# Optimization experiments

Measured on AMD Instinct MI355X. Metric: run time of the kernel, lower is better.

The kernel has to match this reference:

```python
import jax, jax.numpy as jnp
import numpy as np

N_NODES = 50000
N_EDGES = 800000
IN_DIM = 128
HID = 128
N_GRAPHS = 64


def setup_inputs() -> dict:
    key = jax.random.key(0)
    ks = jax.random.split(key, 12)
    edge_index = jax.random.randint(ks[0], (2, N_EDGES), 0, N_NODES, dtype=jnp.int64)
    edge_weight = jax.random.uniform(ks[1], (N_EDGES,), dtype=jnp.float32)
    input_feature = jax.random.normal(ks[2], (N_NODES, IN_DIM), dtype=jnp.float32)
    graph_indicator = jnp.sort(jax.random.randint(ks[3], (N_NODES,), 0, N_GRAPHS, dtype=jnp.int64))
    s = 0.05
    W1 = jax.random.normal(ks[4], (IN_DIM, HID), dtype=jnp.float32) * s
    b1 = jnp.zeros((HID,), jnp.float32)
    W2 = jax.random.normal(ks[5], (HID, HID), dtype=jnp.float32) * s
    b2 = jnp.zeros((HID,), jnp.float32)
    W3 = jax.random.normal(ks[6], (HID, HID), dtype=jnp.float32) * s
    b3 = jnp.zeros((HID,), jnp.float32)
    wa = jax.random.normal(ks[7], (3 * HID, 1), dtype=jnp.float32) * s
    ba = jnp.zeros((1,), jnp.float32)
    Wf = jax.random.normal(ks[8], (3 * HID * 2, IN_DIM), dtype=jnp.float32) * s
    bf = jnp.zeros((IN_DIM,), jnp.float32)
    return dict(edge_index=edge_index, edge_weight=edge_weight,
                input_feature=input_feature, graph_indicator=graph_indicator,
                W1=W1, b1=b1, W2=W2, b2=b2, W3=W3, b3=b3,
                wa=wa, ba=ba, Wf=Wf, bf=bf)


def reference(edge_index, edge_weight, input_feature, graph_indicator,
              W1, b1, W2, b2, W3, b3, wa, ba, Wf, bf):
    src, dst = edge_index[0], edge_index[1]

    def gcn(x, W, b):
        # GraphConvolution: adj @ (x @ W) + b, adj given as weighted edge list
        support = x @ W  # [N, d_out]
        msg = edge_weight[:, None] * support[src]  # [E, d_out] gather
        return jax.ops.segment_sum(msg, dst, num_segments=N_NODES) + b

    g1 = jax.nn.relu(gcn(input_feature, W1, b1))
    g2 = jax.nn.relu(gcn(g1, W2, b2))
    g3 = jax.nn.relu(gcn(g2, W3, b3))
    h = jnp.concatenate([g1, g2, g3], axis=1)  # [N, 3*HID]

    # SelfAttentionPooling: attention score via a 1-dim GraphConvolution, tanh gate
    score = jnp.tanh(gcn(h, wa, ba))  # [N, 1]
    pool = h * score

    # segment avg / max pooling per graph
    seg_sum = jax.ops.segment_sum(pool, graph_indicator, num_segments=N_GRAPHS)
    counts = jax.ops.segment_sum(jnp.ones((N_NODES, 1), pool.dtype), graph_indicator,
                                 num_segments=N_GRAPHS)
    avg = seg_sum / jnp.maximum(counts, 1.0)
    mx = jax.ops.segment_max(pool, graph_indicator, num_segments=N_GRAPHS)
    pooled = jnp.concatenate([avg, mx], axis=1)  # [G, 6*HID]

    return jax.nn.relu(pooled @ Wf + bf)  # [G, IN_DIM]
```

## Files before the change

### kernel.cpp

```cpp
#include <hip/hip_runtime.h>
#include <math.h>

#define HID 128
#define POOL_SEG 16
#define WT_STRIDE 136
#define ELL_D 48
#define SC_CHUNK 2048
#define FXS 16384.0f
#define FXI (1.0f/16384.0f)

typedef __attribute__((ext_vector_type(8))) short short8;
typedef __attribute__((ext_vector_type(4))) float float4v;

__device__ inline short f2bf(float f) {
  unsigned u = __builtin_bit_cast(unsigned, f);
  unsigned r = (u + 0x7fff + ((u >> 16) & 1)) >> 16;
  return (short)r;
}
__device__ inline unsigned pack2bf(float lo, float hi) {
  return (unsigned)(unsigned short)f2bf(lo) | ((unsigned)(unsigned short)f2bf(hi) << 16);
}
__device__ inline float bflo(unsigned u) { return __builtin_bit_cast(float, u << 16); }
__device__ inline float bfhi(unsigned u) { return __builtin_bit_cast(float, u & 0xffff0000u); }
__device__ inline float bf2f(unsigned short s) { return __builtin_bit_cast(float, (unsigned)s << 16); }
__device__ inline unsigned short f2h(float f) {
  _Float16 h = (_Float16)f;
  return __builtin_bit_cast(unsigned short, h);
}
__device__ inline float h2f(unsigned short hb) {
  return (float)__builtin_bit_cast(_Float16, hb);
}

__global__ __launch_bounds__(256) void prologue(
    const void* __restrict__ ei_raw, const float* __restrict__ ew,
    int2* __restrict__ packed,
    const float* __restrict__ W1, const float* __restrict__ W2, const float* __restrict__ W3,
    short* __restrict__ T1, short* __restrict__ T2, short* __restrict__ T3,
    const void* __restrict__ gi_raw, int* __restrict__ gstart,
    int E, int N, int G, int EB) {
  int b = blockIdx.x, t = threadIdx.x;
  if (b < EB) {
    int e = b * 256 + t;
    if (e < E) {
      const int* pw = (const int*)ei_raw;
      int nz = 0;
#pragma unroll
      for (int i = 1; i < 64; i += 2) nz |= pw[i];
      int s, d;
      if (nz == 0) {
        const long long* p = (const long long*)ei_raw;
        s = (int)p[e]; d = (int)p[E + e];
      } else {
        const int* p = (const int*)ei_raw;
        s = p[e]; d = p[E + e];
      }
      packed[e] = make_int2((d << 16) | s, __builtin_bit_cast(int, ew[e]));
    }
  } else if (b < EB + 192) {
    int i = (b - EB) * 256 + t;
    int which = i >> 14, idx = i & 16383;
    int k = idx >> 7, nn = idx & 127;
    const float* W = (which == 0) ? W1 : ((which == 1) ? W2 : W3);
    short* T = (which == 0) ? T1 : ((which == 1) ? T2 : T3);
    T[nn * WT_STRIDE + k] = f2bf(W[idx]);
  } else {
    int g = t;
    if (g > G) return;
    if (g == G) { gstart[g] = N; return; }
    bool is64 = (((const int*)gi_raw)[N - 1] == 0);
    const long long* g64 = (const long long*)gi_raw;
    const int* g32 = (const int*)gi_raw;
    int lo = 0, hi = N;
    while (lo < hi) {
      int mid = (lo + hi) >> 1;
      long long v = is64 ? g64[mid] : (long long)g32[mid];
      if (v < (long long)g) lo = mid + 1; else hi = mid;
    }
    gstart[g] = lo;
  }
}

__global__ void scatter_ell(const int2* __restrict__ packed, int* __restrict__ cursor,
                            unsigned* __restrict__ ell, int E, int N) {
  int group = blockIdx.x & 7;
  int chunk = blockIdx.x >> 3;
  int rng = (N + 7) >> 3;
  int lo = group * rng;
  int hi = lo + rng; if (hi > N) hi = N;
  int base = chunk * SC_CHUNK;
  for (int i = 0; i < SC_CHUNK; i += 256) {
    int e = base + i + threadIdx.x;
    if (e < E) {
      int2 rec = packed[e];
      int d = ((unsigned)rec.x) >> 16;
      if (d >= lo && d < hi) {
        unsigned s = (unsigned)rec.x & 0xFFFFu;
        unsigned short wh = f2h(__builtin_bit_cast(float, rec.y));
        int pos = atomicAdd(&cursor[d], 1);
        if (pos < ELL_D)
          ell[(size_t)d * ELL_D + pos] = (s << 16) | (unsigned)wh;
      }
    }
  }
}

__global__ __launch_bounds__(256) void hist_k(const int* __restrict__ cursor,
                                              int* __restrict__ hist_blk, int n, int nb) {
  __shared__ int lh[ELL_D + 1];
  int t = threadIdx.x;
  if (t <= ELL_D) lh[t] = 0;
  __syncthreads();
  int i = blockIdx.x * 256 + t;
  if (i < n) {
    int d = cursor[i]; if (d > ELL_D) d = ELL_D;
    atomicAdd(&lh[d], 1);
  }
  __syncthreads();
  if (t <= ELL_D) hist_blk[t * nb + blockIdx.x] = lh[t];
}

__global__ __launch_bounds__(64) void scan_k(int* __restrict__ hist_blk, int nb) {
  __shared__ int tot[ELL_D + 1];
  __shared__ int base_s[ELL_D + 1];
  int b = threadIdx.x;
  if (b <= ELL_D) {
    int s = 0;
#pragma unroll 8
    for (int k = 0; k < nb; k++) s += hist_blk[b * nb + k];
    tot[b] = s;
  }
  __syncthreads();
  if (b == 0) {
    int r = 0;
    for (int d = 0; d <= ELL_D; d++) { base_s[d] = r; r += tot[d]; }
  }
  __syncthreads();
  if (b <= ELL_D) {
    int r = base_s[b];
#pragma unroll 8
    for (int k = 0; k < nb; k++) {
      int c = hist_blk[b * nb + k];
      hist_blk[b * nb + k] = r;
      r += c;
    }
  }
}

__global__ __launch_bounds__(256) void gemm_mfma(const float* __restrict__ Af,
                                                 const unsigned short* __restrict__ Abf,
                                                 const short* __restrict__ Wt,
                                                 unsigned short* __restrict__ C,
                                                 int n, int a_is_bf16, int gemm_nb,
                                                 const int* __restrict__ deg,
                                                 const int* __restrict__ hist_blk,
                                                 int* __restrict__ perm, int nb) {
  if (blockIdx.x >= gemm_nb) {
    int blk = blockIdx.x - gemm_nb;
    __shared__ int lcnt[ELL_D + 1];
    __shared__ int lbase[ELL_D + 1];
    int t = threadIdx.x;
    if (t <= ELL_D) {
      lcnt[t] = 0;
      lbase[t] = hist_blk[t * nb + blk];
    }
    __syncthreads();
    int idx = blk * 256 + t;
    int dg = 0, rank = 0;
    if (idx < n) {
      dg = deg[idx]; if (dg > ELL_D) dg = ELL_D;
      rank = atomicAdd(&lcnt[dg], 1);
    }
    __syncthreads();
    if (idx < n) perm[lbase[dg] + rank] = idx;
    return;
  }
  __shared__ short Wlds[128 * WT_STRIDE];
  int t = threadIdx.x;
  {
    const ulonglong2* gsrc = (const ulonglong2*)Wt;
    ulonglong2* ldst = (ulonglong2*)Wlds;
    for (int i = t; i < (128 * WT_STRIDE) / 8; i += 256) ldst[i] = gsrc[i];
  }
  __syncthreads();

  int wave = t >> 6, lane = t & 63;
  int quad = lane >> 4, l15 = lane & 15;
  int m0 = blockIdx.x * 64 + wave * 16;
  size_t SL = (size_t)n * 32;

  int m = m0 + l15; if (m >= n) m = n - 1;
  short8 afrag[4];
  if (a_is_bf16) {
#pragma unroll
    for (int c = 0; c < 4; c++)
      afrag[c] = *(const short8*)(Abf + c * SL + (size_t)m * 32 + quad * 8);
  } else {
    const float* Arow = Af + (size_t)m * 128;
#pragma unroll
    for (int c = 0; c < 4; c++) {
      int k0 = c * 32 + quad * 8;
      float4 x = *(const float4*)(Arow + k0);
      float4 y = *(const float4*)(Arow + k0 + 4);
      short8 a;
      a[0] = f2bf(x.x); a[1] = f2bf(x.y); a[2] = f2bf(x.z); a[3] = f2bf(x.w);
      a[4] = f2bf(y.x); a[5] = f2bf(y.y); a[6] = f2bf(y.z); a[7] = f2bf(y.w);
      afrag[c] = a;
    }
  }

  float4v acc[8];
#pragma unroll
  for (int tt = 0; tt < 8; tt++) acc[tt] = (float4v){0.f, 0.f, 0.f, 0.f};

#pragma unroll
  for (int c = 0; c < 4; c++) {
    int kb = c * 32 + quad * 8;
#pragma unroll
    for (int tt = 0; tt < 8; tt++) {
      const short8* bp = (const short8*)&Wlds[(tt * 16 + l15) * WT_STRIDE + kb];
      acc[tt] = __builtin_amdgcn_mfma_f32_16x16x32_bf16(afrag[c], *bp, acc[tt], 0, 0, 0);
    }
  }

  int rbase = m0 + quad * 4;
#pragma unroll
  for (int tt = 0; tt < 8; tt++) {
    int within = (tt & 1) * 16 + l15;
    size_t sb = (size_t)(tt >> 1) * SL;
#pragma unroll
    for (int r = 0; r < 4; r++) {
      int row = rbase + r;
      if (row < n) C[sb + (size_t)row * 32 + within] = (unsigned short)f2bf(acc[tt][r]);
    }
  }
}

__global__ __launch_bounds__(256) void aggregate_sl(
    const unsigned short* __restrict__ support, const int* __restrict__ deg_arr,
    const unsigned* __restrict__ ell, const float* __restrict__ bias,
    unsigned short* __restrict__ out,
    const unsigned short* __restrict__ g1p, const unsigned short* __restrict__ g2p,
    const float* __restrict__ wa, int* __restrict__ s_pre_fx,
    const int* __restrict__ perm, int n, int do_score) {
  int group = blockIdx.x & 7;
  int slice = group >> 1;
  int chunk = (blockIdx.x >> 3) * 2 + (group & 1);
  int t = threadIdx.x;
  int pos = chunk * 64 + (t >> 2);
  int q = t & 3;
  if (pos >= n) return;
  int node = perm[pos];

  int deg = deg_arr[node]; if (deg > ELL_D) deg = ELL_D;
  const unsigned* row = ell + (size_t)node * ELL_D;
  const uint4* sb = (const uint4*)support + (size_t)slice * n * 4 + q;

  float acc[8];
#pragma unroll
  for (int j = 0; j < 8; j++) acc[j] = 0.f;

  int i = 0;
  for (; i + 3 < deg; i += 4) {
    uint4 rr = *(const uint4*)(row + i);
    float w0 = h2f((unsigned short)(rr.x & 0xFFFF)) * FXS;
    float w1 = h2f((unsigned short)(rr.y & 0xFFFF)) * FXS;
    float w2 = h2f((unsigned short)(rr.z & 0xFFFF)) * FXS;
    float w3 = h2f((unsigned short)(rr.w & 0xFFFF)) * FXS;
    uint4 v0 = sb[(size_t)(rr.x >> 16) * 4];
    uint4 v1 = sb[(size_t)(rr.y >> 16) * 4];
    uint4 v2 = sb[(size_t)(rr.z >> 16) * 4];
    uint4 v3 = sb[(size_t)(rr.w >> 16) * 4];
    acc[0] += rintf(w0 * bflo(v0.x)); acc[1] += rintf(w0 * bfhi(v0.x));
    acc[2] += rintf(w0 * bflo(v0.y)); acc[3] += rintf(w0 * bfhi(v0.y));
    acc[4] += rintf(w0 * bflo(v0.z)); acc[5] += rintf(w0 * bfhi(v0.z));
    acc[6] += rintf(w0 * bflo(v0.w)); acc[7] += rintf(w0 * bfhi(v0.w));
    acc[0] += rintf(w1 * bflo(v1.x)); acc[1] += rintf(w1 * bfhi(v1.x));
    acc[2] += rintf(w1 * bflo(v1.y)); acc[3] += rintf(w1 * bfhi(v1.y));
    acc[4] += rintf(w1 * bflo(v1.z)); acc[5] += rintf(w1 * bfhi(v1.z));
    acc[6] += rintf(w1 * bflo(v1.w)); acc[7] += rintf(w1 * bfhi(v1.w));
    acc[0] += rintf(w2 * bflo(v2.x)); acc[1] += rintf(w2 * bfhi(v2.x));
    acc[2] += rintf(w2 * bflo(v2.y)); acc[3] += rintf(w2 * bfhi(v2.y));
    acc[4] += rintf(w2 * bflo(v2.z)); acc[5] += rintf(w2 * bfhi(v2.z));
    acc[6] += rintf(w2 * bflo(v2.w)); acc[7] += rintf(w2 * bfhi(v2.w));
    acc[0] += rintf(w3 * bflo(v3.x)); acc[1] += rintf(w3 * bfhi(v3.x));
    acc[2] += rintf(w3 * bflo(v3.y)); acc[3] += rintf(w3 * bfhi(v3.y));
    acc[4] += rintf(w3 * bflo(v3.z)); acc[5] += rintf(w3 * bfhi(v3.z));
    acc[6] += rintf(w3 * bflo(v3.w)); acc[7] += rintf(w3 * bfhi(v3.w));
  }
  for (; i < deg; i++) {
    unsigned r0 = row[i];
    float w0 = h2f((unsigned short)(r0 & 0xFFFF)) * FXS;
    uint4 v0 = sb[(size_t)(r0 >> 16) * 4];
    acc[0] += rintf(w0 * bflo(v0.x)); acc[1] += rintf(w0 * bfhi(v0.x));
    acc[2] += rintf(w0 * bflo(v0.y)); acc[3] += rintf(w0 * bfhi(v0.y));
    acc[4] += rintf(w0 * bflo(v0.z)); acc[5] += rintf(w0 * bfhi(v0.z));
    acc[6] += rintf(w0 * bflo(v0.w)); acc[7] += rintf(w0 * bfhi(v0.w));
  }

  float f[8];
#pragma unroll
  for (int j = 0; j < 8; j++) f[j] = acc[j] * FXI;

  float4 b0 = ((const float4*)bias)[slice * 8 + q * 2];
  float4 b1 = ((const float4*)bias)[slice * 8 + q * 2 + 1];
  f[0] = fmaxf(f[0] + b0.x, 0.f); f[1] = fmaxf(f[1] + b0.y, 0.f);
  f[2] = fmaxf(f[2] + b0.z, 0.f); f[3] = fmaxf(f[3] + b0.w, 0.f);
  f[4] = fmaxf(f[4] + b1.x, 0.f); f[5] = fmaxf(f[5] + b1.y, 0.f);
  f[6] = fmaxf(f[6] + b1.z, 0.f); f[7] = fmaxf(f[7] + b1.w, 0.f);

  uint4 o;
  o.x = pack2bf(f[0], f[1]); o.y = pack2bf(f[2], f[3]);
  o.z = pack2bf(f[4], f[5]); o.w = pack2bf(f[6], f[7]);
  ((uint4*)out)[(size_t)slice * n * 4 + (size_t)node * 4 + q] = o;

  if (do_score) {
    uint4 u1 = ((const uint4*)g1p)[(size_t)slice * n * 4 + (size_t)node * 4 + q];
    uint4 u2 = ((const uint4*)g2p)[(size_t)slice * n * 4 + (size_t)node * 4 + q];
    const float* wa1 = wa + slice * 32 + q * 8;
    const float* wa2 = wa1 + 128;
    const float* wa3 = wa1 + 256;
    float sc = bflo(u1.x) * wa1[0] + bfhi(u1.x) * wa1[1]
             + bflo(u1.y) * wa1[2] + bfhi(u1.y) * wa1[3]
             + bflo(u1.z) * wa1[4] + bfhi(u1.z) * wa1[5]
             + bflo(u1.w) * wa1[6] + bfhi(u1.w) * wa1[7]
             + bflo(u2.x) * wa2[0] + bfhi(u2.x) * wa2[1]
             + bflo(u2.y) * wa2[2] + bfhi(u2.y) * wa2[3]
             + bflo(u2.z) * wa2[4] + bfhi(u2.z) * wa2[5]
             + bflo(u2.w) * wa2[6] + bfhi(u2.w) * wa2[7];
#pragma unroll
    for (int j = 0; j < 8; j++) sc += f[j] * wa3[j];
    sc += __shfl_xor(sc, 1, 64);
    sc += __shfl_xor(sc, 2, 64);
    if (q == 0) atomicAdd(&s_pre_fx[node], __float2int_rn(sc * FXS));
  }
}

__global__ __launch_bounds__(384) void pool_partial(const unsigned short* __restrict__ g1,
                                                    const unsigned short* __restrict__ g2,
                                                    const unsigned short* __restrict__ g3,
                                                    const int* __restrict__ s_pre_fx,
                                                    const int* __restrict__ deg_arr,
                                                    const unsigned* __restrict__ ell,
                                                    const float* __restrict__ ba,
                                                    const int* __restrict__ gstart,
                                                    float* __restrict__ part, int n) {
  int g = blockIdx.x / POOL_SEG, seg = blockIdx.x % POOL_SEG;
  int t = threadIdx.x;
  int sg = t >> 7, dd = t & 127;
  const unsigned short* gp = (sg == 0) ? g1 : ((sg == 1) ? g2 : g3);
  const unsigned short* col = gp + (size_t)(dd >> 5) * ((size_t)n * 32) + (dd & 31);
  int s = gstart[g], e = gstart[g + 1];
  int len = e - s;
  int chunk = (len + POOL_SEG - 1) / POOL_SEG;
  int ns = s + seg * chunk;
  int ne = ns + chunk; if (ne > e) ne = e;
  float ba0 = ba[0];
  __shared__ float sc_lds[256];
  float sum = 0.f, mx = -3.402823466e38f;
  for (int tb = ns; tb < ne; tb += 256) {
    int te = tb + 256; if (te > ne) te = ne;
    __syncthreads();
    if (t < te - tb) {
      int node = tb + t;
      int deg = deg_arr[node]; if (deg > ELL_D) deg = ELL_D;
      const unsigned* row = ell + (size_t)node * ELL_D;
      float acc = 0.f;
      for (int i = 0; i < deg; i++) {
        unsigned r = row[i];
        acc += rintf(h2f((unsigned short)(r & 0xFFFF)) * (float)s_pre_fx[r >> 16]);
      }
      sc_lds[t] = tanhf(acc * FXI + ba0);
    }
    __syncthreads();
    for (int node = tb; node < te; node++) {
      float v = bf2f(col[(size_t)node * 32]) * sc_lds[node - tb];
      sum += v;
      mx = fmaxf(mx, v);
    }
  }
  size_t base = (size_t)blockIdx.x * 768;
  part[base + t] = sum;
  part[base + 384 + t] = mx;
}

__global__ __launch_bounds__(512) void tail(const float* __restrict__ part,
                                            const int* __restrict__ gstart,
                                            const float* __restrict__ Wf,
                                            const float* __restrict__ bfb,
                                            float* __restrict__ out) {
  __shared__ float pooled[768];
  __shared__ float red[512];
  int g = blockIdx.x, t = threadIdx.x;
  float cnt = (float)(gstart[g + 1] - gstart[g]);
  float inv = 1.0f / fmaxf(cnt, 1.0f);
  if (t < 384) {
    int d = t;
    float sum = 0.f, mx = -3.402823466e38f;
    for (int seg = 0; seg < POOL_SEG; seg++) {
      size_t base = ((size_t)g * POOL_SEG + seg) * 768;
      sum += part[base + d];
      mx = fmaxf(mx, part[base + 384 + d]);
    }
    pooled[d] = sum * inv;
    pooled[384 + d] = mx;
  }
  __syncthreads();
  int kc = t >> 7, c = t & 127;
  float acc = (kc == 0) ? bfb[c] : 0.f;
  int k0 = kc * 192;
#pragma unroll 8
  for (int k = k0; k < k0 + 192; k++) acc += pooled[k] * Wf[(size_t)k * 128 + c];
  red[t] = acc;
  __syncthreads();
  if (t < 128)
    out[(size_t)g * 128 + t] =
        fmaxf(red[t] + red[t + 128] + red[t + 256] + red[t + 384], 0.f);
}

extern "C" void kernel_launch(void* const* d_in, const int* in_sizes, int n_in,
                              void* d_out, int out_size, void* d_ws, size_t ws_size,
                              hipStream_t stream) {
  const void* ei_raw = d_in[0];
  const float* ew    = (const float*)d_in[1];
  const float* X     = (const float*)d_in[2];
  const void* gi_raw = d_in[3];
  const float* W1 = (const float*)d_in[4];  const float* b1 = (const float*)d_in[5];
  const float* W2 = (const float*)d_in[6];  const float* b2 = (const float*)d_in[7];
  const float* W3 = (const float*)d_in[8];  const float* b3 = (const float*)d_in[9];
  const float* wa = (const float*)d_in[10]; const float* ba = (const float*)d_in[11];
  const float* Wf = (const float*)d_in[12]; const float* bf = (const float*)d_in[13];
  float* out = (float*)d_out;

  const int E = in_sizes[1];
  const int N = in_sizes[2] / 128;
  const int G = out_size / 128;

  char* ws = (char*)d_ws;
  size_t off = 0;
  auto take = [&](size_t bytes) {
    char* p = ws + off;
    off = (off + bytes + 255) & ~(size_t)255;
    return p;
  };
  const int NB256 = (N + 255) / 256;
  int* zb = (int*)take((size_t)N * 8);
  int* cursor   = zb;
  int* s_pre_fx = zb + N;
  int* hist_blk = (int*)take((size_t)(ELL_D + 1) * NB256 * 4);
  int* perm     = (int*)take((size_t)N * 4);
  int2* packed  = (int2*)take((size_t)E * 8);
  unsigned* ell = (unsigned*)take((size_t)N * ELL_D * 4);
  short*    wt1 = (short*)take((size_t)128 * WT_STRIDE * 2);
  short*    wt2 = (short*)take((size_t)128 * WT_STRIDE * 2);
  short*    wt3 = (short*)take((size_t)128 * WT_STRIDE * 2);
  unsigned short* support = (unsigned short*)take((size_t)N * 128 * 2);
  unsigned short* g1      = (unsigned short*)take((size_t)N * 128 * 2);
  unsigned short* g2      = (unsigned short*)take((size_t)N * 128 * 2);
  unsigned short* g3      = (unsigned short*)take((size_t)N * 128 * 2);
  int*   gstart  = (int*)take((size_t)(G + 1) * 4);
  float* part    = (float*)take((size_t)G * POOL_SEG * 768 * 4);
  if (off > ws_size) return;

  hipMemsetAsync(zb, 0, (size_t)N * 8, stream);

  const int EB = (E + 255) / 256;
  prologue<<<EB + 192 + 1, 256, 0, stream>>>(ei_raw, ew, packed,
                                             W1, W2, W3, wt1, wt2, wt3,
                                             gi_raw, gstart, E, N, G, EB);
  {
    int chunks = (E + SC_CHUNK - 1) / SC_CHUNK;
    scatter_ell<<<8 * chunks, 256, 0, stream>>>(packed, cursor, ell, E, N);
  }
  hist_k<<<NB256, 256, 0, stream>>>(cursor, hist_blk, N, NB256);
  scan_k<<<1, 64, 0, stream>>>(hist_blk, NB256);

  const int GB = (N + 63) / 64;
  const int NB64 = (N + 63) / 64;
  const int AGB = 8 * ((NB64 + 1) / 2);
  gemm_mfma<<<GB + NB256, 256, 0, stream>>>(X, (const unsigned short*)nullptr, wt1,
                                            support, N, 0, GB, cursor, hist_blk, perm, NB256);
  aggregate_sl<<<AGB, 256, 0, stream>>>(support, cursor, ell, b1, g1,
                                        nullptr, nullptr, nullptr, nullptr, perm, N, 0);
  gemm_mfma<<<GB, 256, 0, stream>>>((const float*)nullptr, g1, wt2, support, N, 1, GB,
                                    nullptr, nullptr, nullptr, 0);
  aggregate_sl<<<AGB, 256, 0, stream>>>(support, cursor, ell, b2, g2,
                                        nullptr, nullptr, nullptr, nullptr, perm, N, 0);
  gemm_mfma<<<GB, 256, 0, stream>>>((const float*)nullptr, g2, wt3, support, N, 1, GB,
                                    nullptr, nullptr, nullptr, 0);
  aggregate_sl<<<AGB, 256, 0, stream>>>(support, cursor, ell, b3, g3,
                                        g1, g2, wa, s_pre_fx, perm, N, 1);

  pool_partial<<<G * POOL_SEG, 384, 0, stream>>>(g1, g2, g3, s_pre_fx, cursor, ell,
                                                 ba, gstart, part, N);
  tail<<<G, 512, 0, stream>>>(part, gstart, Wf, bf, out);
}
```

Before: 343.4 us.

## Use 16-column feature slices and drop degree-sorted node permutation

Feature matrices move from four 32-column slices to eight 16-column slices. Each node row in a slice is now 32 bytes, so every random gather in aggregation touches a smaller footprint and each slice's working set fits better in cache. The degree histogram, scan and permutation kernels are removed, and aggregation now walks nodes in natural order with two threads per node. This saves two launches and the perm indirection, at the cost of more load imbalance across nodes of different degree within a wave.

```diff
diff --git a/kernel.cpp b/kernel.cpp
--- a/kernel.cpp
+++ b/kernel.cpp
@@ -104,76 +104,11 @@
   }
 }
 
-__global__ __launch_bounds__(256) void hist_k(const int* __restrict__ cursor,
-                                              int* __restrict__ hist_blk, int n, int nb) {
-  __shared__ int lh[ELL_D + 1];
-  int t = threadIdx.x;
-  if (t <= ELL_D) lh[t] = 0;
-  __syncthreads();
-  int i = blockIdx.x * 256 + t;
-  if (i < n) {
-    int d = cursor[i]; if (d > ELL_D) d = ELL_D;
-    atomicAdd(&lh[d], 1);
-  }
-  __syncthreads();
-  if (t <= ELL_D) hist_blk[t * nb + blockIdx.x] = lh[t];
-}
-
-__global__ __launch_bounds__(64) void scan_k(int* __restrict__ hist_blk, int nb) {
-  __shared__ int tot[ELL_D + 1];
-  __shared__ int base_s[ELL_D + 1];
-  int b = threadIdx.x;
-  if (b <= ELL_D) {
-    int s = 0;
-#pragma unroll 8
-    for (int k = 0; k < nb; k++) s += hist_blk[b * nb + k];
-    tot[b] = s;
-  }
-  __syncthreads();
-  if (b == 0) {
-    int r = 0;
-    for (int d = 0; d <= ELL_D; d++) { base_s[d] = r; r += tot[d]; }
-  }
-  __syncthreads();
-  if (b <= ELL_D) {
-    int r = base_s[b];
-#pragma unroll 8
-    for (int k = 0; k < nb; k++) {
-      int c = hist_blk[b * nb + k];
-      hist_blk[b * nb + k] = r;
-      r += c;
-    }
-  }
-}
-
 __global__ __launch_bounds__(256) void gemm_mfma(const float* __restrict__ Af,
                                                  const unsigned short* __restrict__ Abf,
                                                  const short* __restrict__ Wt,
                                                  unsigned short* __restrict__ C,
-                                                 int n, int a_is_bf16, int gemm_nb,
-                                                 const int* __restrict__ deg,
-                                                 const int* __restrict__ hist_blk,
-                                                 int* __restrict__ perm, int nb) {
-  if (blockIdx.x >= gemm_nb) {
-    int blk = blockIdx.x - gemm_nb;
-    __shared__ int lcnt[ELL_D + 1];
-    __shared__ int lbase[ELL_D + 1];
-    int t = threadIdx.x;
-    if (t <= ELL_D) {
-      lcnt[t] = 0;
-      lbase[t] = hist_blk[t * nb + blk];
-    }
-    __syncthreads();
-    int idx = blk * 256 + t;
-    int dg = 0, rank = 0;
-    if (idx < n) {
-      dg = deg[idx]; if (dg > ELL_D) dg = ELL_D;
-      rank = atomicAdd(&lcnt[dg], 1);
-    }
-    __syncthreads();
-    if (idx < n) perm[lbase[dg] + rank] = idx;
-    return;
-  }
+                                                 int n, int a_is_bf16) {
   __shared__ short Wlds[128 * WT_STRIDE];
   int t = threadIdx.x;
   {
@@ -186,14 +121,16 @@
   int wave = t >> 6, lane = t & 63;
   int quad = lane >> 4, l15 = lane & 15;
   int m0 = blockIdx.x * 64 + wave * 16;
-  size_t SL = (size_t)n * 32;
+  size_t SL8 = (size_t)n * 16;
 
   int m = m0 + l15; if (m >= n) m = n - 1;
   short8 afrag[4];
   if (a_is_bf16) {
 #pragma unroll
-    for (int c = 0; c < 4; c++)
-      afrag[c] = *(const short8*)(Abf + c * SL + (size_t)m * 32 + quad * 8);
+    for (int c = 0; c < 4; c++) {
+      int k0 = c * 32 + quad * 8;
+      afrag[c] = *(const short8*)(Abf + (size_t)(k0 >> 4) * SL8 + (size_t)m * 16 + (k0 & 15));
+    }
   } else {
     const float* Arow = Af + (size_t)m * 128;
 #pragma unroll
@@ -225,12 +162,11 @@
   int rbase = m0 + quad * 4;
 #pragma unroll
   for (int tt = 0; tt < 8; tt++) {
-    int within = (tt & 1) * 16 + l15;
-    size_t sb = (size_t)(tt >> 1) * SL;
+    size_t sb = (size_t)tt * SL8;
 #pragma unroll
     for (int r = 0; r < 4; r++) {
       int row = rbase + r;
-      if (row < n) C[sb + (size_t)row * 32 + within] = (unsigned short)f2bf(acc[tt][r]);
+      if (row < n) C[sb + (size_t)row * 16 + l15] = (unsigned short)f2bf(acc[tt][r]);
     }
   }
 }
@@ -241,19 +177,16 @@
     unsigned short* __restrict__ out,
     const unsigned short* __restrict__ g1p, const unsigned short* __restrict__ g2p,
     const float* __restrict__ wa, int* __restrict__ s_pre_fx,
-    const int* __restrict__ perm, int n, int do_score) {
-  int group = blockIdx.x & 7;
-  int slice = group >> 1;
-  int chunk = (blockIdx.x >> 3) * 2 + (group & 1);
+    int n, int do_score) {
+  int slice = blockIdx.x & 7;
   int t = threadIdx.x;
-  int pos = chunk * 64 + (t >> 2);
-  int q = t & 3;
-  if (pos >= n) return;
-  int node = perm[pos];
+  int node = (blockIdx.x >> 3) * 128 + (t >> 1);
+  int q = t & 1;
+  if (node >= n) return;
 
   int deg = deg_arr[node]; if (deg > ELL_D) deg = ELL_D;
   const unsigned* row = ell + (size_t)node * ELL_D;
-  const uint4* sb = (const uint4*)support + (size_t)slice * n * 4 + q;
+  const uint4* sb = (const uint4*)support + (size_t)slice * n * 2 + q;
 
   float acc[8];
 #pragma unroll
@@ -266,10 +199,10 @@
     float w1 = h2f((unsigned short)(rr.y & 0xFFFF)) * FXS;
     float w2 = h2f((unsigned short)(rr.z & 0xFFFF)) * FXS;
     float w3 = h2f((unsigned short)(rr.w & 0xFFFF)) * FXS;
-    uint4 v0 = sb[(size_t)(rr.x >> 16) * 4];
-    uint4 v1 = sb[(size_t)(rr.y >> 16) * 4];
-    uint4 v2 = sb[(size_t)(rr.z >> 16) * 4];
-    uint4 v3 = sb[(size_t)(rr.w >> 16) * 4];
+    uint4 v0 = sb[(size_t)(rr.x >> 16) * 2];
+    uint4 v1 = sb[(size_t)(rr.y >> 16) * 2];
+    uint4 v2 = sb[(size_t)(rr.z >> 16) * 2];
+    uint4 v3 = sb[(size_t)(rr.w >> 16) * 2];
     acc[0] += rintf(w0 * bflo(v0.x)); acc[1] += rintf(w0 * bfhi(v0.x));
     acc[2] += rintf(w0 * bflo(v0.y)); acc[3] += rintf(w0 * bfhi(v0.y));
     acc[4] += rintf(w0 * bflo(v0.z)); acc[5] += rintf(w0 * bfhi(v0.z));
@@ -290,7 +223,7 @@
   for (; i < deg; i++) {
     unsigned r0 = row[i];
     float w0 = h2f((unsigned short)(r0 & 0xFFFF)) * FXS;
-    uint4 v0 = sb[(size_t)(r0 >> 16) * 4];
+    uint4 v0 = sb[(size_t)(r0 >> 16) * 2];
     acc[0] += rintf(w0 * bflo(v0.x)); acc[1] += rintf(w0 * bfhi(v0.x));
     acc[2] += rintf(w0 * bflo(v0.y)); acc[3] += rintf(w0 * bfhi(v0.y));
     acc[4] += rintf(w0 * bflo(v0.z)); acc[5] += rintf(w0 * bfhi(v0.z));
@@ -301,8 +234,8 @@
 #pragma unroll
   for (int j = 0; j < 8; j++) f[j] = acc[j] * FXI;
 
-  float4 b0 = ((const float4*)bias)[slice * 8 + q * 2];
-  float4 b1 = ((const float4*)bias)[slice * 8 + q * 2 + 1];
+  float4 b0 = ((const float4*)bias)[slice * 4 + q * 2];
+  float4 b1 = ((const float4*)bias)[slice * 4 + q * 2 + 1];
   f[0] = fmaxf(f[0] + b0.x, 0.f); f[1] = fmaxf(f[1] + b0.y, 0.f);
   f[2] = fmaxf(f[2] + b0.z, 0.f); f[3] = fmaxf(f[3] + b0.w, 0.f);
   f[4] = fmaxf(f[4] + b1.x, 0.f); f[5] = fmaxf(f[5] + b1.y, 0.f);
@@ -311,12 +244,12 @@
   uint4 o;
   o.x = pack2bf(f[0], f[1]); o.y = pack2bf(f[2], f[3]);
   o.z = pack2bf(f[4], f[5]); o.w = pack2bf(f[6], f[7]);
-  ((uint4*)out)[(size_t)slice * n * 4 + (size_t)node * 4 + q] = o;
+  ((uint4*)out)[(size_t)slice * n * 2 + (size_t)node * 2 + q] = o;
 
   if (do_score) {
-    uint4 u1 = ((const uint4*)g1p)[(size_t)slice * n * 4 + (size_t)node * 4 + q];
-    uint4 u2 = ((const uint4*)g2p)[(size_t)slice * n * 4 + (size_t)node * 4 + q];
-    const float* wa1 = wa + slice * 32 + q * 8;
+    uint4 u1 = ((const uint4*)g1p)[(size_t)slice * n * 2 + (size_t)node * 2 + q];
+    uint4 u2 = ((const uint4*)g2p)[(size_t)slice * n * 2 + (size_t)node * 2 + q];
+    const float* wa1 = wa + slice * 16 + q * 8;
     const float* wa2 = wa1 + 128;
     const float* wa3 = wa1 + 256;
     float sc = bflo(u1.x) * wa1[0] + bfhi(u1.x) * wa1[1]
@@ -330,7 +263,6 @@
 #pragma unroll
     for (int j = 0; j < 8; j++) sc += f[j] * wa3[j];
     sc += __shfl_xor(sc, 1, 64);
-    sc += __shfl_xor(sc, 2, 64);
     if (q == 0) atomicAdd(&s_pre_fx[node], __float2int_rn(sc * FXS));
   }
 }
@@ -348,7 +280,7 @@
   int t = threadIdx.x;
   int sg = t >> 7, dd = t & 127;
   const unsigned short* gp = (sg == 0) ? g1 : ((sg == 1) ? g2 : g3);
-  const unsigned short* col = gp + (size_t)(dd >> 5) * ((size_t)n * 32) + (dd & 31);
+  const unsigned short* col = gp + (size_t)(dd >> 4) * ((size_t)n * 16) + (dd & 15);
   int s = gstart[g], e = gstart[g + 1];
   int len = e - s;
   int chunk = (len + POOL_SEG - 1) / POOL_SEG;
@@ -373,7 +305,7 @@
     }
     __syncthreads();
     for (int node = tb; node < te; node++) {
-      float v = bf2f(col[(size_t)node * 32]) * sc_lds[node - tb];
+      float v = bf2f(col[(size_t)node * 16]) * sc_lds[node - tb];
       sum += v;
       mx = fmaxf(mx, v);
     }
@@ -442,12 +374,9 @@
     off = (off + bytes + 255) & ~(size_t)255;
     return p;
   };
-  const int NB256 = (N + 255) / 256;
   int* zb = (int*)take((size_t)N * 8);
   int* cursor   = zb;
   int* s_pre_fx = zb + N;
-  int* hist_blk = (int*)take((size_t)(ELL_D + 1) * NB256 * 4);
-  int* perm     = (int*)take((size_t)N * 4);
   int2* packed  = (int2*)take((size_t)E * 8);
   unsigned* ell = (unsigned*)take((size_t)N * ELL_D * 4);
   short*    wt1 = (short*)take((size_t)128 * WT_STRIDE * 2);
@@ -471,24 +400,18 @@
     int chunks = (E + SC_CHUNK - 1) / SC_CHUNK;
     scatter_ell<<<8 * chunks, 256, 0, stream>>>(packed, cursor, ell, E, N);
   }
-  hist_k<<<NB256, 256, 0, stream>>>(cursor, hist_blk, N, NB256);
-  scan_k<<<1, 64, 0, stream>>>(hist_blk, NB256);
 
   const int GB = (N + 63) / 64;
-  const int NB64 = (N + 63) / 64;
-  const int AGB = 8 * ((NB64 + 1) / 2);
-  gemm_mfma<<<GB + NB256, 256, 0, stream>>>(X, (const unsigned short*)nullptr, wt1,
-                                            support, N, 0, GB, cursor, hist_blk, perm, NB256);
+  const int AGB = 8 * ((N + 127) / 128);
+  gemm_mfma<<<GB, 256, 0, stream>>>(X, (const unsigned short*)nullptr, wt1, support, N, 0);
   aggregate_sl<<<AGB, 256, 0, stream>>>(support, cursor, ell, b1, g1,
-                                        nullptr, nullptr, nullptr, nullptr, perm, N, 0);
-  gemm_mfma<<<GB, 256, 0, stream>>>((const float*)nullptr, g1, wt2, support, N, 1, GB,
-                                    nullptr, nullptr, nullptr, 0);
+                                        nullptr, nullptr, nullptr, nullptr, N, 0);
+  gemm_mfma<<<GB, 256, 0, stream>>>((const float*)nullptr, g1, wt2, support, N, 1);
   aggregate_sl<<<AGB, 256, 0, stream>>>(support, cursor, ell, b2, g2,
-                                        nullptr, nullptr, nullptr, nullptr, perm, N, 0);
-  gemm_mfma<<<GB, 256, 0, stream>>>((const float*)nullptr, g2, wt3, support, N, 1, GB,
-                                    nullptr, nullptr, nullptr, 0);
+                                        nullptr, nullptr, nullptr, nullptr, N, 0);
+  gemm_mfma<<<GB, 256, 0, stream>>>((const float*)nullptr, g2, wt3, support, N, 1);
   aggregate_sl<<<AGB, 256, 0, stream>>>(support, cursor, ell, b3, g3,
-                                        g1, g2, wa, s_pre_fx, perm, N, 1);
+                                        g1, g2, wa, s_pre_fx, N, 1);
 
   pool_partial<<<G * POOL_SEG, 384, 0, stream>>>(g1, g2, g3, s_pre_fx, cursor, ell,
                                                  ba, gstart, part, N);
```

Result: slower. 371.5 us (+8.2%).
